# Kernel tuning notes

Measured on AMD Instinct MI355X. Metric: run time of the kernel, lower is better.

The kernel has to match this reference:

```python
import jax, jax.numpy as jnp
import numpy as np

N_QUBITS = 4  # matches init n_qubits; depth = 1


def _apply_rx(state, angles, wire):
    # state: (B, 2**N) complex64; angles: (B,) real. RX(theta) = [[c, -is],[-is, c]], c=cos(t/2), s=sin(t/2)
    B = state.shape[0]
    left = 2 ** wire
    st = state.reshape(B, left, 2, -1)
    half = angles * 0.5
    c = jnp.cos(half).astype(jnp.complex64).reshape(B, 1, 1)
    s = ((-1j) * jnp.sin(half).astype(jnp.complex64)).reshape(B, 1, 1)
    s0 = st[:, :, 0, :]
    s1 = st[:, :, 1, :]
    out = jnp.stack([c * s0 + s * s1, s * s0 + c * s1], axis=2)
    return out.reshape(B, -1)


def _apply_cnot(state, ctrl):
    # CNOT on wires [ctrl, ctrl+1]: flip target amplitudes where control bit is 1
    B = state.shape[0]
    left = 2 ** ctrl
    st = state.reshape(B, left, 2, 2, -1)
    st = st.at[:, :, 1, :, :].set(st[:, :, 1, ::-1, :])
    return st.reshape(B, -1)


def _qgate(angles, theta):
    # angles: (B, N_QUBITS) data-encoded RX angles; theta: (N_QUBITS,) trainable RX angles
    # Circuit: RX(data) on each wire -> CNOT chain -> RX(theta) on each wire -> <Z_i> per wire
    B = angles.shape[0]
    state = jnp.zeros((B, 2 ** N_QUBITS), jnp.complex64).at[:, 0].set(1.0 + 0.0j)
    for i in range(N_QUBITS):
        state = _apply_rx(state, angles[:, i], i)
    for i in range(N_QUBITS - 1):
        state = _apply_cnot(state, i)
    for i in range(N_QUBITS):
        state = _apply_rx(state, jnp.broadcast_to(theta[i], (B,)), i)
    probs = jnp.real(state * jnp.conj(state)).reshape((B,) + (2,) * N_QUBITS)
    expz = []
    for i in range(N_QUBITS):
        axes = tuple(a for a in range(1, N_QUBITS + 1) if a != i + 1)
        p = probs.sum(axis=axes)  # (B, 2)
        expz.append(p[:, 0] - p[:, 1])
    return jnp.stack(expz, axis=1)  # (B, N_QUBITS)


def setup_inputs() -> dict:
    key = jax.random.key(0)
    ks = jax.random.split(key, 16)
    T, B, D, H, Q = 256, 512, 128, 128, N_QUBITS

    def w(k, shape, scale=0.05):
        return jax.random.normal(k, shape, jnp.float32) * scale

    inp = {
        'inputs': jax.random.normal(ks[0], (T, B, D), jnp.float32),
        'hx0': jnp.zeros((B, H), jnp.float32),
        'cx0': jnp.zeros((B, H), jnp.float32),
    }
    for j, n in enumerate(['f', 'i', 'g', 'o']):
        inp['W' + n] = w(ks[1 + j], (H, D + H))
        inp['b' + n] = jnp.zeros((H,), jnp.float32)
        inp['W' + n + 'q'] = w(ks[5 + j], (Q, D + H))
        inp['b' + n + 'q'] = jnp.zeros((Q,), jnp.float32)
        inp['th' + n] = jax.random.normal(ks[9 + j], (Q,), jnp.float32)
    inp['Wq'] = w(ks[13], (H, Q))
    inp['bq'] = jnp.zeros((H,), jnp.float32)
    return inp


def reference(inputs, hx0, cx0, Wf, bf, Wfq, bfq, thf, Wi, bi, Wiq, biq, thi,
              Wg, bg, Wgq, bgq, thg, Wo, bo, Woq, boq, tho, Wq, bq):
    def step(carry, x):
        hx, cx = carry
        comb = jnp.concatenate([x, hx], axis=1)  # (B, D+H)

        def lin(W, b):
            return comb @ W.T + b

        def qg(Wl, bl, th):
            return _qgate(lin(Wl, bl), th) @ Wq.T + bq

        f = jax.nn.sigmoid(lin(Wf, bf)) + jax.nn.sigmoid(qg(Wfq, bfq, thf))
        i = jax.nn.sigmoid(lin(Wi, bi)) + jax.nn.sigmoid(qg(Wiq, biq, thi))
        g = jnp.tanh(lin(Wg, bg)) + jnp.tanh(qg(Wgq, bgq, thg))
        o = jax.nn.sigmoid(lin(Wo, bo)) + jax.nn.sigmoid(qg(Woq, boq, tho))
        cx2 = f * cx + i * g
        hx2 = o * jnp.tanh(cx2)
        return (hx2, cx2), hx2

    (hxT, cxT), outs = jax.lax.scan(step, (hx0, cx0), inputs)
    return outs, (hxT, cxT)
```

## Files before the change

### kernel.cpp

```cpp
#include <hip/hip_runtime.h>
#include <cmath>

#define TT 256
#define BB 512
#define DD 128
#define HH 128
#define NCOL 528
#define KK 256
#define NCPAD 576

__global__ __launch_bounds__(256) void pack_weights(
    const float* __restrict__ Wf, const float* __restrict__ bf,
    const float* __restrict__ Wfq, const float* __restrict__ bfq,
    const float* __restrict__ Wi, const float* __restrict__ bi,
    const float* __restrict__ Wiq, const float* __restrict__ biq,
    const float* __restrict__ Wg, const float* __restrict__ bg,
    const float* __restrict__ Wgq, const float* __restrict__ bgq,
    const float* __restrict__ Wo, const float* __restrict__ bo,
    const float* __restrict__ Woq, const float* __restrict__ boq,
    float* __restrict__ Wxp, float* __restrict__ Whr3,
    float* __restrict__ Whql, float* __restrict__ bcat)
{
    int idx = blockIdx.x * blockDim.x + threadIdx.x;
    if (idx < NCOL * KK) {
        int c = idx >> 8, k = idx & 255;
        const float* srcW; int cl;
        if (c < 512) { int g = c >> 7; cl = c & 127;
            srcW = (g == 0) ? Wf : (g == 1) ? Wi : (g == 2) ? Wg : Wo; }
        else { int g = (c - 512) >> 2; cl = (c - 512) & 3;
            srcW = (g == 0) ? Wfq : (g == 1) ? Wiq : (g == 2) ? Wgq : Woq; }
        float v = srcW[(size_t)cl * KK + k];
        if (k < 128) Wxp[(size_t)c * 128 + k] = v;
        else {
            int kk = k - 128;
            if (c < 512) {
                int gate = c >> 7, hcol = c & 127;
                int t = hcol * 4 + (kk >> 5);
                int j = gate * 8 + ((kk >> 2) & 7);
                Whr3[((size_t)j * 512 + t) * 4 + (kk & 3)] = v;
            } else {
                Whql[(size_t)(c - 512) * 128 + kk] = v;
            }
        }
    }
    if (idx < NCPAD) {
        float b = 0.f;
        int c = idx;
        if (c < 512) { int g = c >> 7; int cl = c & 127;
            b = (g == 0) ? bf[cl] : (g == 1) ? bi[cl] : (g == 2) ? bg[cl] : bo[cl]; }
        else if (c < NCOL) { int g = (c - 512) >> 2; int cl = (c - 512) & 3;
            b = (g == 0) ? bfq[cl] : (g == 1) ? biq[cl] : (g == 2) ? bgq[cl] : boq[cl]; }
        bcat[c] = b;
    }
}

#define P1_BM 128
#define P1_BN 64
#define ATP 132
#define BTP 68
__global__ __launch_bounds__(256, 3) void xgemm(
    const float* __restrict__ X, const float* __restrict__ Wxp,
    const float* __restrict__ bcat, float* __restrict__ Zx)
{
    __shared__ float At[64][ATP];
    __shared__ float Bt[64][BTP];
    const int tid = threadIdx.x;
    const int m0 = blockIdx.x * P1_BM;
    const int c0 = blockIdx.y * P1_BN;
    const int tm = tid >> 3;
    const int tn = tid & 7;
    float acc[4][8] = {};

    for (int khf = 0; khf < 2; ++khf) {
        #pragma unroll
        for (int j = 0; j < 8; ++j) {
            int fidx = tid + 256 * j;
            int m = fidx >> 4, k4 = (fidx & 15) * 4;
            float4 v = *(const float4*)(X + (size_t)(m0 + m) * 128 + khf * 64 + k4);
            At[k4 + 0][m] = v.x; At[k4 + 1][m] = v.y; At[k4 + 2][m] = v.z; At[k4 + 3][m] = v.w;
        }
        #pragma unroll
        for (int j = 0; j < 4; ++j) {
            int fidx = tid + 256 * j;
            int c = fidx >> 4, k4 = (fidx & 15) * 4;
            int cg = c0 + c;
            float4 v = make_float4(0.f, 0.f, 0.f, 0.f);
            if (cg < NCOL) v = *(const float4*)(Wxp + (size_t)cg * 128 + khf * 64 + k4);
            Bt[k4 + 0][c] = v.x; Bt[k4 + 1][c] = v.y; Bt[k4 + 2][c] = v.z; Bt[k4 + 3][c] = v.w;
        }
        __syncthreads();
        #pragma unroll 4
        for (int k = 0; k < 64; ++k) {
            float4 a  = *(const float4*)&At[k][tm * 4];
            float4 b0 = *(const float4*)&Bt[k][tn * 8];
            float4 b1 = *(const float4*)&Bt[k][tn * 8 + 4];
            float av[4] = {a.x, a.y, a.z, a.w};
            float bv[8] = {b0.x, b0.y, b0.z, b0.w, b1.x, b1.y, b1.z, b1.w};
            #pragma unroll
            for (int i = 0; i < 4; ++i)
                #pragma unroll
                for (int j = 0; j < 8; ++j)
                    acc[i][j] = fmaf(av[i], bv[j], acc[i][j]);
        }
        __syncthreads();
    }
    int c = c0 + tn * 8;
    if (c < NCOL) {
        float4 ba = *(const float4*)(bcat + c);
        float4 bb = *(const float4*)(bcat + c + 4);
        #pragma unroll
        for (int i = 0; i < 4; ++i) {
            int m = m0 + tm * 4 + i;
            float4 o0, o1;
            o0.x = acc[i][0] + ba.x; o0.y = acc[i][1] + ba.y;
            o0.z = acc[i][2] + ba.z; o0.w = acc[i][3] + ba.w;
            o1.x = acc[i][4] + bb.x; o1.y = acc[i][5] + bb.y;
            o1.z = acc[i][6] + bb.z; o1.w = acc[i][7] + bb.w;
            *(float4*)(Zx + (size_t)m * NCOL + c)     = o0;
            *(float4*)(Zx + (size_t)m * NCOL + c + 4) = o1;
        }
    }
}

__device__ __forceinline__ float sigm(float x) { return 1.0f / (1.0f + __expf(-x)); }
__device__ __forceinline__ float tanh_f(float x) {
    float e = __expf(2.f * x);
    return 1.f - 2.f / (e + 1.f);
}

#define FMA4(acc, Wv, Xv) acc = fmaf((Wv).x, (Xv).x, fmaf((Wv).y, (Xv).y, fmaf((Wv).z, (Xv).z, fmaf((Wv).w, (Xv).w, (acc)))))
#define PIN4(Wv) asm volatile("" : "+v"((Wv).x), "+v"((Wv).y), "+v"((Wv).z), "+v"((Wv).w))

__device__ __forceinline__ int hsk(int k) { return k + 8 * (k >> 5); }

__global__ __launch_bounds__(512)
__attribute__((amdgpu_waves_per_eu(2, 2)))
void qlstm_rec(
    const float* __restrict__ Zx,
    const float* __restrict__ Whr3,
    const float* __restrict__ Whql,
    const float* __restrict__ hx0, const float* __restrict__ cx0,
    float* __restrict__ stateH, float* __restrict__ stateC,
    const float* __restrict__ Wq, const float* __restrict__ bq,
    const float* __restrict__ thf, const float* __restrict__ thi,
    const float* __restrict__ thg, const float* __restrict__ tho,
    float* __restrict__ out, int t0, int TC)
{
    __shared__ __align__(16) float hL[2][152];
    __shared__ __align__(16) float WhqL[16][132];
    __shared__ __align__(16) float EZ[2][4][4];

    const int tid  = threadIdx.x;
    const int row0 = blockIdx.x * 2;
    const int ks   = tid & 3;
    const int h    = tid >> 2;

    float4 wv[32];
    const float4* Wp3 = (const float4*)Whr3;
    #pragma unroll
    for (int j = 0; j < 32; ++j) wv[j] = Wp3[j * 512 + tid];
    #pragma unroll
    for (int j = 0; j < 32; ++j) PIN4(wv[j]);

    #pragma unroll
    for (int j = 0; j < 4; ++j) {
        int i = tid * 4 + j;
        WhqL[i >> 7][i & 127] = Whql[i];
    }

    const bool isCell = (ks < 2);
    const int  r      = ks & 1;
    float4 wqv = make_float4(0.f, 0.f, 0.f, 0.f);
    float bb = 0.f, cxr = 0.f;
    if (isCell) {
        wqv = *(const float4*)(Wq + h * 4);
        bb  = bq[h];
    }
    int qc = 0, rq = 0, kseg = 0, qw = 0, qg = 0;
    float qcoef = 1.f, qth3 = 0.f;
    if (tid < 128) {
        qc = tid >> 3; rq = (tid >> 2) & 1; kseg = tid & 3;
        qg = qc >> 2;  qw = qc & 3;
        const float* thp = (qg == 0) ? thf : (qg == 1) ? thi : (qg == 2) ? thg : tho;
        qcoef = (qw < 3) ? cosf(thp[qw]) : 1.f;
        qth3  = thp[3];
    }
    if (isCell) {
        const float* hs = (t0 == 0) ? hx0 : stateH;
        const float* cs = (t0 == 0) ? cx0 : stateC;
        hL[r][hsk(h)] = hs[(size_t)(row0 + r) * HH + h];
        cxr           = cs[(size_t)(row0 + r) * HH + h];
    }
    __syncthreads();

    for (int tc = 0; tc < TC; ++tc) {
        const float* zrow = Zx + ((size_t)tc * BB + row0) * NCOL;
        float zc0 = 0, zc1 = 0, zc2 = 0, zc3 = 0, zqv = 0;
        if (isCell) {
            const float* zp = zrow + (size_t)r * NCOL + h;
            zc0 = zp[0]; zc1 = zp[128]; zc2 = zp[256]; zc3 = zp[384];
        }
        if (tid < 128) zqv = zrow[(size_t)rq * NCOL + 512 + qc];

        float aF0 = 0, aF1 = 0, aI0 = 0, aI1 = 0, aG0 = 0, aG1 = 0, aO0 = 0, aO1 = 0;
        {
            const float4* h0p = (const float4*)&hL[0][40 * ks];
            const float4* h1p = (const float4*)&hL[1][40 * ks];
            #pragma unroll
            for (int k4 = 0; k4 < 8; ++k4) {
                float4 hv0 = h0p[k4];
                float4 hv1 = h1p[k4];
                FMA4(aF0, wv[k4],      hv0);  FMA4(aF1, wv[k4],      hv1);
                FMA4(aI0, wv[8 + k4],  hv0);  FMA4(aI1, wv[8 + k4],  hv1);
                FMA4(aG0, wv[16 + k4], hv0);  FMA4(aG1, wv[16 + k4], hv1);
                FMA4(aO0, wv[24 + k4], hv0);  FMA4(aO1, wv[24 + k4], hv1);
            }
        }
        #define BRED(v) { v += __shfl_xor(v, 1, 64); v += __shfl_xor(v, 2, 64); }
        BRED(aF0) BRED(aF1) BRED(aI0) BRED(aI1)
        BRED(aG0) BRED(aG1) BRED(aO0) BRED(aO1)
        #undef BRED

        if (tid < 128) {
            float qa = 0.f;
            const float4* hqp = (const float4*)&hL[rq][40 * kseg];
            #pragma unroll
            for (int k4 = 0; k4 < 8; ++k4) {
                float4 wq4 = *(const float4*)&WhqL[qc][kseg * 32 + 4 * k4];
                FMA4(qa, wq4, hqp[k4]);
            }
            qa += __shfl_xor(qa, 1, 64);
            qa += __shfl_xor(qa, 2, 64);
            float a = zqv + qa;
            float c = __cosf(a);
            int lbase = ((qg & 1) * 4) * 8 + rq * 4;
            float cw0 = __shfl(c, lbase, 64);
            float cw1 = __shfl(c, lbase + 8, 64);
            float cw2 = __shfl(c, lbase + 16, 64);
            float own = (qw == 3) ? __cosf(a + qth3) : c;
            float prod = 1.f;
            if (qw >= 1) prod *= cw0;
            if (qw >= 2) prod *= cw1;
            if (qw == 3) prod *= cw2;
            if (kseg == 0) EZ[rq][qg][qw] = qcoef * prod * own;
        }
        __syncthreads();

        if (isCell) {
            float pf = zc0 + (r ? aF1 : aF0);
            float pi = zc1 + (r ? aI1 : aI0);
            float pg = zc2 + (r ? aG1 : aG0);
            float po = zc3 + (r ? aO1 : aO0);
            float4 Ef = *(const float4*)&EZ[r][0][0];
            float4 Ei = *(const float4*)&EZ[r][1][0];
            float4 Eg = *(const float4*)&EZ[r][2][0];
            float4 Eo = *(const float4*)&EZ[r][3][0];
            float qf = fmaf(Ef.x, wqv.x, fmaf(Ef.y, wqv.y, fmaf(Ef.z, wqv.z, fmaf(Ef.w, wqv.w, bb))));
            float qi = fmaf(Ei.x, wqv.x, fmaf(Ei.y, wqv.y, fmaf(Ei.z, wqv.z, fmaf(Ei.w, wqv.w, bb))));
            float qg2 = fmaf(Eg.x, wqv.x, fmaf(Eg.y, wqv.y, fmaf(Eg.z, wqv.z, fmaf(Eg.w, wqv.w, bb))));
            float qo = fmaf(Eo.x, wqv.x, fmaf(Eo.y, wqv.y, fmaf(Eo.z, wqv.z, fmaf(Eo.w, wqv.w, bb))));
            float f  = sigm(pf)   + sigm(qf);
            float ii = sigm(pi)   + sigm(qi);
            float gg = tanh_f(pg) + tanh_f(qg2);
            float oo = sigm(po)   + sigm(qo);
            float cn = fmaf(f, cxr, ii * gg);
            cxr = cn;
            float hn = oo * tanh_f(cn);
            hL[r][hsk(h)] = hn;
            out[((size_t)(t0 + tc) * BB + row0 + r) * HH + h] = hn;
        }
        __syncthreads();
    }

    if (isCell) {
        float hn = hL[r][hsk(h)];
        stateH[(size_t)(row0 + r) * HH + h] = hn;
        stateC[(size_t)(row0 + r) * HH + h] = cxr;
        if (t0 + TC == TT) {
            size_t base = (size_t)TT * BB * HH;
            out[base + (size_t)(row0 + r) * HH + h]                   = hn;
            out[base + (size_t)BB * HH + (size_t)(row0 + r) * HH + h] = cxr;
        }
    }
}

extern "C" void kernel_launch(void* const* d_in, const int* in_sizes, int n_in,
                              void* d_out, int out_size, void* d_ws, size_t ws_size,
                              hipStream_t stream) {
    const float* X   = (const float*)d_in[0];
    const float* hx0 = (const float*)d_in[1];
    const float* cx0 = (const float*)d_in[2];
    const float* Wf  = (const float*)d_in[3];
    const float* bf  = (const float*)d_in[4];
    const float* Wfq = (const float*)d_in[5];
    const float* bfq = (const float*)d_in[6];
    const float* thf = (const float*)d_in[7];
    const float* Wi  = (const float*)d_in[8];
    const float* bi  = (const float*)d_in[9];
    const float* Wiq = (const float*)d_in[10];
    const float* biq = (const float*)d_in[11];
    const float* thi = (const float*)d_in[12];
    const float* Wg  = (const float*)d_in[13];
    const float* bg  = (const float*)d_in[14];
    const float* Wgq = (const float*)d_in[15];
    const float* bgq = (const float*)d_in[16];
    const float* thg = (const float*)d_in[17];
    const float* Wo  = (const float*)d_in[18];
    const float* bo  = (const float*)d_in[19];
    const float* Woq = (const float*)d_in[20];
    const float* boq = (const float*)d_in[21];
    const float* tho = (const float*)d_in[22];
    const float* Wq  = (const float*)d_in[23];
    const float* bq  = (const float*)d_in[24];

    float* ws = (float*)d_ws;
    float* Wxp    = ws;
    float* Whr3   = Wxp + 528 * 128;
    float* Whql   = Whr3 + 65536;
    float* bcatp  = Whql + 2048;
    float* stateH = bcatp + NCPAD;
    float* stateC = stateH + 512 * 128;
    float* Zxb    = stateC + 512 * 128;

    size_t fixed_bytes = (size_t)(Zxb - ws) * sizeof(float);
    int TC = 256;
    while (TC > 4 && fixed_bytes + (size_t)TC * 512 * NCOL * 4 > ws_size) TC >>= 1;

    pack_weights<<<(NCOL * KK + 255) / 256, 256, 0, stream>>>(
        Wf, bf, Wfq, bfq, Wi, bi, Wiq, biq, Wg, bg, Wgq, bgq, Wo, bo, Woq, boq,
        Wxp, Whr3, Whql, bcatp);

    for (int t0 = 0; t0 < TT; t0 += TC) {
        xgemm<<<dim3(TC * 512 / P1_BM, NCPAD / P1_BN), 256, 0, stream>>>(
            X + (size_t)t0 * BB * DD, Wxp, bcatp, Zxb);
        qlstm_rec<<<256, 512, 0, stream>>>(
            Zxb, Whr3, Whql, hx0, cx0, stateH, stateC, Wq, bq,
            thf, thi, thg, tho, (float*)d_out, t0, TC);
    }
}
```

Baseline: 767.9 us.

## Fuse quantum-gate projection into main matvec loop with DPP reductions

Moves the Whq dot product for the quantum gate angles from a separate shared-memory pass over the first 128 threads into the main recurrent FMA loop. It is spread across 128 threads with weights held in registers, reusing the h vectors already loaded from LDS. Shuffle-based quad reductions become DPP row-permute adds. The cross-wire cosine products now happen in the cell threads from two small LDS arrays instead of via shuffles. The goal is a shorter serial critical path per timestep, at the cost of more registers per thread (32 extra floats) under a fixed two-waves occupancy constraint, which could cause spills.

New measurement: 774.0 us. No clear change (+0.8%).

```diff
diff --git a/kernel.cpp b/kernel.cpp
--- a/kernel.cpp
+++ b/kernel.cpp
@@ -131,6 +131,10 @@
 #define FMA4(acc, Wv, Xv) acc = fmaf((Wv).x, (Xv).x, fmaf((Wv).y, (Xv).y, fmaf((Wv).z, (Xv).z, fmaf((Wv).w, (Xv).w, (acc)))))
 #define PIN4(Wv) asm volatile("" : "+v"((Wv).x), "+v"((Wv).y), "+v"((Wv).z), "+v"((Wv).w))
 
+#define DPPRED(v) { \
+    v += __int_as_float(__builtin_amdgcn_update_dpp(0, __float_as_int(v), 0xB1, 0xF, 0xF, true)); \
+    v += __int_as_float(__builtin_amdgcn_update_dpp(0, __float_as_int(v), 0x4E, 0xF, 0xF, true)); }
+
 __device__ __forceinline__ int hsk(int k) { return k + 8 * (k >> 5); }
 
 __global__ __launch_bounds__(512)
@@ -147,26 +151,20 @@
     float* __restrict__ out, int t0, int TC)
 {
     __shared__ __align__(16) float hL[2][152];
-    __shared__ __align__(16) float WhqL[16][132];
-    __shared__ __align__(16) float EZ[2][4][4];
+    __shared__ __align__(16) float cEd[2][20];
+    __shared__ __align__(16) float cEc[2][20];
 
     const int tid  = threadIdx.x;
     const int row0 = blockIdx.x * 2;
     const int ks   = tid & 3;
     const int h    = tid >> 2;
 
+    const float4* Wp3 = (const float4*)Whr3;
     float4 wv[32];
-    const float4* Wp3 = (const float4*)Whr3;
     #pragma unroll
     for (int j = 0; j < 32; ++j) wv[j] = Wp3[j * 512 + tid];
     #pragma unroll
     for (int j = 0; j < 32; ++j) PIN4(wv[j]);
-
-    #pragma unroll
-    for (int j = 0; j < 4; ++j) {
-        int i = tid * 4 + j;
-        WhqL[i >> 7][i & 127] = Whql[i];
-    }
 
     const bool isCell = (ks < 2);
     const int  r      = ks & 1;
@@ -176,14 +174,19 @@
         wqv = *(const float4*)(Wq + h * 4);
         bb  = bq[h];
     }
-    int qc = 0, rq = 0, kseg = 0, qw = 0, qg = 0;
+    const bool isQ = (tid & 15) < 4;
+    const int qi = tid >> 4;
+    const int rq = qi & 1, qc = qi >> 1;
+    const int qg = qc >> 2, qw = qc & 3;
     float qcoef = 1.f, qth3 = 0.f;
-    if (tid < 128) {
-        qc = tid >> 3; rq = (tid >> 2) & 1; kseg = tid & 3;
-        qg = qc >> 2;  qw = qc & 3;
+    float4 qw4[8] = {};
+    if (isQ) {
         const float* thp = (qg == 0) ? thf : (qg == 1) ? thi : (qg == 2) ? thg : tho;
         qcoef = (qw < 3) ? cosf(thp[qw]) : 1.f;
         qth3  = thp[3];
+        const float4* qp = (const float4*)(Whql + (size_t)qc * 128 + ks * 32);
+        #pragma unroll
+        for (int j = 0; j < 8; ++j) qw4[j] = qp[j];
     }
     if (isCell) {
         const float* hs = (t0 == 0) ? hx0 : stateH;
@@ -200,9 +203,10 @@
             const float* zp = zrow + (size_t)r * NCOL + h;
             zc0 = zp[0]; zc1 = zp[128]; zc2 = zp[256]; zc3 = zp[384];
         }
-        if (tid < 128) zqv = zrow[(size_t)rq * NCOL + 512 + qc];
+        if (isQ) zqv = zrow[(size_t)rq * NCOL + 512 + qc];
 
         float aF0 = 0, aF1 = 0, aI0 = 0, aI1 = 0, aG0 = 0, aG1 = 0, aO0 = 0, aO1 = 0;
+        float qa = 0.f;
         {
             const float4* h0p = (const float4*)&hL[0][40 * ks];
             const float4* h1p = (const float4*)&hL[1][40 * ks];
@@ -214,35 +218,24 @@
                 FMA4(aI0, wv[8 + k4],  hv0);  FMA4(aI1, wv[8 + k4],  hv1);
                 FMA4(aG0, wv[16 + k4], hv0);  FMA4(aG1, wv[16 + k4], hv1);
                 FMA4(aO0, wv[24 + k4], hv0);  FMA4(aO1, wv[24 + k4], hv1);
+                float4 hq;
+                hq.x = rq ? hv1.x : hv0.x; hq.y = rq ? hv1.y : hv0.y;
+                hq.z = rq ? hv1.z : hv0.z; hq.w = rq ? hv1.w : hv0.w;
+                FMA4(qa, qw4[k4], hq);
             }
         }
-        #define BRED(v) { v += __shfl_xor(v, 1, 64); v += __shfl_xor(v, 2, 64); }
-        BRED(aF0) BRED(aF1) BRED(aI0) BRED(aI1)
-        BRED(aG0) BRED(aG1) BRED(aO0) BRED(aO1)
-        #undef BRED
-
-        if (tid < 128) {
-            float qa = 0.f;
-            const float4* hqp = (const float4*)&hL[rq][40 * kseg];
-            #pragma unroll
-            for (int k4 = 0; k4 < 8; ++k4) {
-                float4 wq4 = *(const float4*)&WhqL[qc][kseg * 32 + 4 * k4];
-                FMA4(qa, wq4, hqp[k4]);
-            }
-            qa += __shfl_xor(qa, 1, 64);
-            qa += __shfl_xor(qa, 2, 64);
+        DPPRED(aF0) DPPRED(aF1) DPPRED(aI0) DPPRED(aI1)
+        DPPRED(aG0) DPPRED(aG1) DPPRED(aO0) DPPRED(aO1)
+        DPPRED(qa)
+
+        if (isQ) {
             float a = zqv + qa;
             float c = __cosf(a);
-            int lbase = ((qg & 1) * 4) * 8 + rq * 4;
-            float cw0 = __shfl(c, lbase, 64);
-            float cw1 = __shfl(c, lbase + 8, 64);
-            float cw2 = __shfl(c, lbase + 16, 64);
-            float own = (qw == 3) ? __cosf(a + qth3) : c;
-            float prod = 1.f;
-            if (qw >= 1) prod *= cw0;
-            if (qw >= 2) prod *= cw1;
-            if (qw == 3) prod *= cw2;
-            if (kseg == 0) EZ[rq][qg][qw] = qcoef * prod * own;
+            float dval = (qw < 3) ? qcoef * c : __cosf(a + qth3);
+            if (ks == 0) {
+                cEd[rq][qc] = dval;
+                cEc[rq][qc] = c;
+            }
         }
         __syncthreads();
 
@@ -251,18 +244,22 @@
             float pi = zc1 + (r ? aI1 : aI0);
             float pg = zc2 + (r ? aG1 : aG0);
             float po = zc3 + (r ? aO1 : aO0);
-            float4 Ef = *(const float4*)&EZ[r][0][0];
-            float4 Ei = *(const float4*)&EZ[r][1][0];
-            float4 Eg = *(const float4*)&EZ[r][2][0];
-            float4 Eo = *(const float4*)&EZ[r][3][0];
-            float qf = fmaf(Ef.x, wqv.x, fmaf(Ef.y, wqv.y, fmaf(Ef.z, wqv.z, fmaf(Ef.w, wqv.w, bb))));
-            float qi = fmaf(Ei.x, wqv.x, fmaf(Ei.y, wqv.y, fmaf(Ei.z, wqv.z, fmaf(Ei.w, wqv.w, bb))));
-            float qg2 = fmaf(Eg.x, wqv.x, fmaf(Eg.y, wqv.y, fmaf(Eg.z, wqv.z, fmaf(Eg.w, wqv.w, bb))));
-            float qo = fmaf(Eo.x, wqv.x, fmaf(Eo.y, wqv.y, fmaf(Eo.z, wqv.z, fmaf(Eo.w, wqv.w, bb))));
-            float f  = sigm(pf)   + sigm(qf);
-            float ii = sigm(pi)   + sigm(qi);
-            float gg = tanh_f(pg) + tanh_f(qg2);
-            float oo = sigm(po)   + sigm(qo);
+            float qz[4];
+            #pragma unroll
+            for (int g = 0; g < 4; ++g) {
+                float4 dv = *(const float4*)&cEd[r][g * 4];
+                float4 cv = *(const float4*)&cEc[r][g * 4];
+                float c01  = cv.x * cv.y;
+                float c012 = c01 * cv.z;
+                qz[g] = fmaf(dv.x, wqv.x,
+                        fmaf(dv.y * cv.x, wqv.y,
+                        fmaf(dv.z * c01, wqv.z,
+                        fmaf(dv.w * c012, wqv.w, bb))));
+            }
+            float f  = sigm(pf)   + sigm(qz[0]);
+            float ii = sigm(pi)   + sigm(qz[1]);
+            float gg = tanh_f(pg) + tanh_f(qz[2]);
+            float oo = sigm(po)   + sigm(qz[3]);
             float cn = fmaf(f, cxr, ii * gg);
             cxr = cn;
             float hn = oo * tanh_f(cn);
```
